# Optimization experiments

Measured on AMD Instinct MI355X. Metric: run time of the kernel, lower is better.

Reference implementation:

```python
import jax, jax.numpy as jnp
import numpy as np

THRESH = 0.33
EPS = 1e-10


def _ternarize(x, max_val):
    # x / (max(|x|)+eps) thresholded to {-1, 0, +1}
    n = x / (max_val + EPS)
    return jnp.where(n > THRESH, 1, jnp.where(n < -THRESH, -1, 0)).astype(jnp.int32)


def setup_inputs() -> dict:
    key = jax.random.key(0)
    k1, k2 = jax.random.split(key)
    V, D = 131072, 1024
    qs = jax.random.normal(k1, (D,), dtype=jnp.float32)
    # embedding init: xavier-ish normal + small noise, then row-normalized (as in _initialize_embeddings)
    W = jax.random.normal(k2, (V, D), dtype=jnp.float32)
    W = W / jnp.linalg.norm(W, axis=1, keepdims=True)
    return {"quantum_state": qs, "embedding_weight": W, "top_k": 16}


def reference(quantum_state, embedding_weight, top_k):
    V, D = embedding_weight.shape
    # --- coarse pass: ternary quantization of query and full table ---
    t_state = _ternarize(quantum_state, jnp.max(jnp.abs(quantum_state)))          # [D]
    t_emb = _ternarize(embedding_weight,
                       jnp.max(jnp.abs(embedding_weight), axis=1, keepdims=True))  # [V,D]
    eq = (t_state[None, :] == t_emb)                                               # [V,D]
    # matches contribute +1, mismatches -0.5 (matches.sum - 0.5*mismatches.sum)
    ternary_sim = jnp.sum(jnp.where(eq, 1.0, -0.5), axis=1)                        # [V]
    k3 = min(top_k * 3, V)
    _, top_ternary_idx = jax.lax.top_k(ternary_sim, k3)                            # [k3]
    # --- refine pass: cosine similarity on candidates ---
    cand = embedding_weight[top_ternary_idx]                                       # [k3,D]
    q_n = quantum_state / (jnp.linalg.norm(quantum_state) + 1e-12)
    c_n = cand / (jnp.linalg.norm(cand, axis=1, keepdims=True) + 1e-12)
    refined = c_n @ q_n                                                            # [k3]
    top_scores, top_local = jax.lax.top_k(refined, top_k)                          # [top_k]
    top_global = top_ternary_idx[top_local]
    return top_scores, top_global
```

## Files before the change

### kernel.cpp

```cpp
#include <hip/hip_runtime.h>
#include <stdint.h>

#define VROWS 131072
#define DIM   1024
#define TTHRESH 0.33f
#define TEPS    1e-10f
#define KB_BLOCKS 2048
#define REG_BLOCKS 832
#define NSB   32
#define CAP   16384
#define CAPL  4096

#define MBOUND ((double)TTHRESH + 0x1p-26)

#define CTRS_OFF  1024
#define MATCH_OFF 4096
#define PART_OFF  (MATCH_OFF + 4 * VROWS)
#define KEYS_OFF  ((PART_OFF + 4 * NSB * 1025 + 7) & ~7)

typedef float f32x4 __attribute__((ext_vector_type(4)));

__device__ __forceinline__ float max4abs(f32x4 a) {
    return fmaxf(fmaxf(fabsf(a.x), fabsf(a.y)), fmaxf(fabsf(a.z), fabsf(a.w)));
}

__device__ __forceinline__ float boundary(float d) {
    double md = MBOUND * (double)d;
    float r = (float)md;
    if (!((double)r >= md)) r = __int_as_float(__float_as_int(r) + 1);
    return r;
}

#define SLOT(x, j) { \
    unsigned long long bp = __ballot((x) >= r); \
    unsigned long long bn = __ballot((x) <= nr); \
    unsigned long long b0 = ~(bp | bn); \
    cnt += (int)__popcll((bp & MP[j]) | (bn & MN[j]) | (b0 & ~(MP[j] | MN[j]))); }

template <bool NT>
__device__ __forceinline__ f32x4 ldW(const f32x4* p) {
    if (NT) return __builtin_nontemporal_load(p);
    return *p;
}

template <bool NT>
__device__ __forceinline__ void rows16(const float* __restrict__ W, int row0, int lane,
                                       const unsigned long long* MP, const unsigned long long* MN,
                                       int* __restrict__ matches) {
    const f32x4* p = (const f32x4*)(W + (size_t)row0 * DIM) + lane;
    f32x4 c0 = ldW<NT>(p), c1 = ldW<NT>(p + 64), c2 = ldW<NT>(p + 128), c3 = ldW<NT>(p + 192);
    f32x4 n0 = c0, n1 = c1, n2 = c2, n3 = c3;
#pragma unroll 1
    for (int i = 0; i < 16; ++i) {
        if (i < 15) {
            const f32x4* pn = (const f32x4*)(W + (size_t)(row0 + i + 1) * DIM) + lane;
            n0 = ldW<NT>(pn); n1 = ldW<NT>(pn + 64); n2 = ldW<NT>(pn + 128); n3 = ldW<NT>(pn + 192);
        }
        float m = fmaxf(fmaxf(max4abs(c0), max4abs(c1)), fmaxf(max4abs(c2), max4abs(c3)));
        for (int s = 1; s < 64; s <<= 1) m = fmaxf(m, __shfl_xor(m, s));
        float r = boundary(m + TEPS), nr = -r;
        int cnt = 0;
        SLOT(c0.x, 0)  SLOT(c0.y, 1)  SLOT(c0.z, 2)  SLOT(c0.w, 3)
        SLOT(c1.x, 4)  SLOT(c1.y, 5)  SLOT(c1.z, 6)  SLOT(c1.w, 7)
        SLOT(c2.x, 8)  SLOT(c2.y, 9)  SLOT(c2.z, 10) SLOT(c2.w, 11)
        SLOT(c3.x, 12) SLOT(c3.y, 13) SLOT(c3.z, 14) SLOT(c3.w, 15)
        if (lane == 0) matches[row0 + i] = cnt;
        c0 = n0; c1 = n1; c2 = n2; c3 = n3;
    }
}

__global__ __launch_bounds__(256, 8) void kB_coarse(const float* __restrict__ W,
                                                    const float* __restrict__ q,
                                                    int* __restrict__ matches) {
    int t = threadIdx.x;
    int wave = t >> 6, lane = t & 63;

    const f32x4* q4 = (const f32x4*)q;
    f32x4 qv0 = q4[lane], qv1 = q4[64 + lane], qv2 = q4[128 + lane], qv3 = q4[192 + lane];
    float mq = fmaxf(fmaxf(max4abs(qv0), max4abs(qv1)), fmaxf(max4abs(qv2), max4abs(qv3)));
    for (int s = 1; s < 64; s <<= 1) mq = fmaxf(mq, __shfl_xor(mq, s));
    float rq = boundary(mq + TEPS), nrq = -rq;
    unsigned long long MP[16], MN[16];
#pragma unroll
    for (int j = 0; j < 4; ++j) {
        f32x4 v = (j == 0) ? qv0 : (j == 1) ? qv1 : (j == 2) ? qv2 : qv3;
        MP[j * 4 + 0] = __ballot(v.x >= rq);  MN[j * 4 + 0] = __ballot(v.x <= nrq);
        MP[j * 4 + 1] = __ballot(v.y >= rq);  MN[j * 4 + 1] = __ballot(v.y <= nrq);
        MP[j * 4 + 2] = __ballot(v.z >= rq);  MN[j * 4 + 2] = __ballot(v.z <= nrq);
        MP[j * 4 + 3] = __ballot(v.w >= rq);  MN[j * 4 + 3] = __ballot(v.w <= nrq);
    }

    int bb = (blockIdx.x * 997) & (KB_BLOCKS - 1);
    int row0 = bb * 64 + wave * 16;
    if (bb < REG_BLOCKS) {
        rows16<false>(W, row0, lane, MP, MN, matches);
    } else {
        rows16<true>(W, row0, lane, MP, MN, matches);
    }
}

__global__ __launch_bounds__(1024) void kHist(const int* __restrict__ matches,
                                              int* __restrict__ partials,
                                              int* __restrict__ ctrs) {
    __shared__ int h[1025];
    int t = threadIdx.x;
    if (t == 0) h[1024] = 0;
    if (blockIdx.x == 0 && t < 2) ctrs[t] = 0;
    h[t] = 0;
    __syncthreads();
    int gid = blockIdx.x * 1024 + t;
    int4 m4 = ((const int4*)matches)[gid];
    atomicAdd(&h[m4.x], 1);
    atomicAdd(&h[m4.y], 1);
    atomicAdd(&h[m4.z], 1);
    atomicAdd(&h[m4.w], 1);
    __syncthreads();
    int* dst = partials + blockIdx.x * 1025;
    dst[t] = h[t];
    if (t == 0) dst[1024] = h[1024];
}

__global__ __launch_bounds__(1024) void kGF(const float* __restrict__ W,
                                            const float* __restrict__ q,
                                            const int* __restrict__ topk,
                                            const int* __restrict__ matches,
                                            const int* __restrict__ partials,
                                            unsigned long long* __restrict__ keys,
                                            int* __restrict__ ctrs,
                                            float* __restrict__ out) {
    __shared__ int S[2048];
    __shared__ __align__(16) float qs[DIM];
    __shared__ float redf[1024];
    __shared__ unsigned long long kl[CAPL];
    __shared__ int sel[192];
    __shared__ float refined[192];
    __shared__ int sT, sWin, sG;
    __shared__ float sQn;
    int t = threadIdx.x;
    int b = blockIdx.x;
    int* gcount = &ctrs[0];
    int* done2 = &ctrs[1];

    int K = *topk;
    if (K < 1) K = 1;
    if (K > 64) K = 64;
    int k3 = 3 * K;
    if (k3 > VROWS) k3 = VROWS;

    int hb = 0, hb1 = 0;
    for (int k = 0; k < NSB; ++k) {
        hb += partials[k * 1025 + t];
        if (t == 0) hb1 += partials[k * 1025 + 1024];
    }
    S[t] = hb;
    S[1024 + t] = (t == 0) ? hb1 : 0;
    __syncthreads();

    for (int s = 1; s < 2048; s <<= 1) {
        int a = S[t] + ((t + s < 2048) ? S[t + s] : 0);
        int bsum = S[1024 + t] + ((1024 + t + s < 2048) ? S[1024 + t + s] : 0);
        __syncthreads();
        S[t] = a;
        S[1024 + t] = bsum;
        __syncthreads();
    }
    if (S[t] >= k3 && S[t + 1] < k3) sT = t;
    if (t == 0 && S[1024] >= k3) sT = 1024;
    __syncthreads();
    int T = sT;

    int gid = b * 1024 + t;
    int4 m4 = ((const int4*)matches)[gid];
    int rbase = gid * 4;
    if (m4.x >= T) { int p = atomicAdd(gcount, 1); if (p < CAP) keys[p] = ((unsigned long long)m4.x << 32) | (unsigned int)(~(rbase)); }
    if (m4.y >= T) { int p = atomicAdd(gcount, 1); if (p < CAP) keys[p] = ((unsigned long long)m4.y << 32) | (unsigned int)(~(rbase + 1)); }
    if (m4.z >= T) { int p = atomicAdd(gcount, 1); if (p < CAP) keys[p] = ((unsigned long long)m4.z << 32) | (unsigned int)(~(rbase + 2)); }
    if (m4.w >= T) { int p = atomicAdd(gcount, 1); if (p < CAP) keys[p] = ((unsigned long long)m4.w << 32) | (unsigned int)(~(rbase + 3)); }

    __threadfence();
    if (t == 0) sWin = atomicAdd(done2, 1);
    __syncthreads();
    if (sWin != NSB - 1) return;
    __threadfence();

    if (t < 256) ((float4*)qs)[t] = ((const float4*)q)[t];
    __syncthreads();
    float qv = qs[t];
    redf[t] = qv * qv;
    __syncthreads();
    for (int s = 512; s > 0; s >>= 1) {
        if (t < s) redf[t] += redf[t + s];
        __syncthreads();
    }
    if (t == 0) sQn = sqrtf(redf[0]) + 1e-12f;

    int G = atomicAdd(gcount, 0);
    if (G <= CAPL) {
        for (int i = t; i < G; i += 1024) kl[i] = keys[i];
        if (t == 0) sG = G;
    } else {
        if (t == 0) {
            int n = 0;
            for (int v = 0; v < VROWS && n < k3; ++v)
                if (matches[v] > T) kl[n++] = ((unsigned long long)matches[v] << 32) | (unsigned int)(~v);
            for (int v = 0; v < VROWS && n < k3; ++v)
                if (matches[v] == T) kl[n++] = ((unsigned long long)matches[v] << 32) | (unsigned int)(~v);
            sG = n;
        }
    }
    __syncthreads();
    G = sG;

    for (int i = t; i < G; i += 1024) {
        unsigned long long ki = kl[i];
        int rank = 0;
        for (int j = 0; j < G; ++j) rank += (kl[j] > ki) ? 1 : 0;
        if (rank < k3) sel[rank] = (int)(~(unsigned int)ki);
    }
    __syncthreads();

    int wave = t >> 6, lane = t & 63;
    float qn = sQn;
    for (int i = wave; i < k3; i += 16) {
        int row = sel[i];
        const float4* Wr = (const float4*)(W + (size_t)row * DIM);
        float dot = 0.f, ss = 0.f;
        for (int j2 = 0; j2 < 4; ++j2) {
            float4 a = Wr[j2 * 64 + lane];
            float4 bq = ((const float4*)qs)[j2 * 64 + lane];
            dot += a.x * bq.x + a.y * bq.y + a.z * bq.z + a.w * bq.w;
            ss  += a.x * a.x + a.y * a.y + a.z * a.z + a.w * a.w;
        }
        for (int s = 1; s < 64; s <<= 1) {
            dot += __shfl_xor(dot, s);
            ss  += __shfl_xor(ss, s);
        }
        if (lane == 0) refined[i] = dot / ((sqrtf(ss) + 1e-12f) * qn);
    }
    __syncthreads();

    if (t < k3) {
        float rv = refined[t];
        int rank = 0;
        for (int j = 0; j < k3; ++j)
            rank += ((refined[j] > rv) || (refined[j] == rv && j < t)) ? 1 : 0;
        if (rank < K) {
            out[rank] = rv;
            out[K + rank] = (float)sel[t];
        }
    }
}

extern "C" void kernel_launch(void* const* d_in, const int* in_sizes, int n_in,
                              void* d_out, int out_size, void* d_ws, size_t ws_size,
                              hipStream_t stream) {
    const float* q = (const float*)d_in[0];
    const float* W = (const float*)d_in[1];
    const int* topk = (const int*)d_in[2];
    float* out = (float*)d_out;
    char* ws = (char*)d_ws;

    int* ctrs = (int*)(ws + CTRS_OFF);
    int* matches = (int*)(ws + MATCH_OFF);
    int* partials = (int*)(ws + PART_OFF);
    unsigned long long* keys = (unsigned long long*)(ws + KEYS_OFF);

    kB_coarse<<<KB_BLOCKS, 256, 0, stream>>>(W, q, matches);
    kHist<<<NSB, 1024, 0, stream>>>(matches, partials, ctrs);
    kGF<<<NSB, 1024, 0, stream>>>(W, q, topk, matches, partials, keys, ctrs, out);
}
```

Before: 116.4 us.

## Use per-block local thresholds for candidate gathering; split final refine into its own kernel

Each histogram block now computes its own top-k3 threshold from its local histogram and gathers candidates directly. This removes the global partial-histogram reduction and the last-block-wins atomic election. The refine and top-k work moves to a separate single-block kernel that reads the gathered keys. A local threshold yields a superset of the true candidates, so the final rank step may process more keys (up to about 32·k3), and it falls back to ranking straight from global memory when the key count exceeds the LDS capacity.

```diff
diff --git a/kernel.cpp b/kernel.cpp
--- a/kernel.cpp
+++ b/kernel.cpp
@@ -15,8 +15,7 @@
 
 #define CTRS_OFF  1024
 #define MATCH_OFF 4096
-#define PART_OFF  (MATCH_OFF + 4 * VROWS)
-#define KEYS_OFF  ((PART_OFF + 4 * NSB * 1025 + 7) & ~7)
+#define KEYS_OFF  (MATCH_OFF + 4 * VROWS)
 
 typedef float f32x4 __attribute__((ext_vector_type(4)));
 
@@ -71,9 +70,11 @@
 
 __global__ __launch_bounds__(256, 8) void kB_coarse(const float* __restrict__ W,
                                                     const float* __restrict__ q,
-                                                    int* __restrict__ matches) {
+                                                    int* __restrict__ matches,
+                                                    int* __restrict__ ctrs) {
     int t = threadIdx.x;
     int wave = t >> 6, lane = t & 63;
+    if (blockIdx.x == 0 && t < 2) ctrs[t] = 0;
 
     const f32x4* q4 = (const f32x4*)q;
     f32x4 qv0 = q4[lane], qv1 = q4[64 + lane], qv2 = q4[128 + lane], qv3 = q4[192 + lane];
@@ -99,47 +100,81 @@
     }
 }
 
-__global__ __launch_bounds__(1024) void kHist(const int* __restrict__ matches,
-                                              int* __restrict__ partials,
-                                              int* __restrict__ ctrs) {
+__global__ __launch_bounds__(1024) void kLG(const int* __restrict__ matches,
+                                            const int* __restrict__ topk,
+                                            unsigned long long* __restrict__ keys,
+                                            int* __restrict__ gcount) {
     __shared__ int h[1025];
+    __shared__ int S[2048];
+    __shared__ int sT;
     int t = threadIdx.x;
+    int b = blockIdx.x;
+
+    int K = *topk;
+    if (K < 1) K = 1;
+    if (K > 64) K = 64;
+    int k3 = 3 * K;
+    if (k3 > VROWS) k3 = VROWS;
+
     if (t == 0) h[1024] = 0;
-    if (blockIdx.x == 0 && t < 2) ctrs[t] = 0;
     h[t] = 0;
     __syncthreads();
-    int gid = blockIdx.x * 1024 + t;
+    int gid = b * 1024 + t;
     int4 m4 = ((const int4*)matches)[gid];
     atomicAdd(&h[m4.x], 1);
     atomicAdd(&h[m4.y], 1);
     atomicAdd(&h[m4.z], 1);
     atomicAdd(&h[m4.w], 1);
     __syncthreads();
-    int* dst = partials + blockIdx.x * 1025;
-    dst[t] = h[t];
-    if (t == 0) dst[1024] = h[1024];
-}
-
-__global__ __launch_bounds__(1024) void kGF(const float* __restrict__ W,
-                                            const float* __restrict__ q,
-                                            const int* __restrict__ topk,
-                                            const int* __restrict__ matches,
-                                            const int* __restrict__ partials,
-                                            unsigned long long* __restrict__ keys,
-                                            int* __restrict__ ctrs,
-                                            float* __restrict__ out) {
-    __shared__ int S[2048];
+
+    S[t] = h[t];
+    S[1024 + t] = (t == 0) ? h[1024] : 0;
+    __syncthreads();
+    for (int s = 1; s < 2048; s <<= 1) {
+        int a = S[t] + ((t + s < 2048) ? S[t + s] : 0);
+        int bsum = S[1024 + t] + ((1024 + t + s < 2048) ? S[1024 + t + s] : 0);
+        __syncthreads();
+        S[t] = a;
+        S[1024 + t] = bsum;
+        __syncthreads();
+    }
+    if (S[t] >= k3 && S[t + 1] < k3) sT = t;
+    if (t == 0 && S[1024] >= k3) sT = 1024;
+    __syncthreads();
+    int T = sT;
+
+    int rbase = gid * 4;
+    if (m4.x >= T) { int p = atomicAdd(gcount, 1); if (p < CAP) keys[p] = ((unsigned long long)m4.x << 32) | (unsigned int)(~(rbase)); }
+    if (m4.y >= T) { int p = atomicAdd(gcount, 1); if (p < CAP) keys[p] = ((unsigned long long)m4.y << 32) | (unsigned int)(~(rbase + 1)); }
+    if (m4.z >= T) { int p = atomicAdd(gcount, 1); if (p < CAP) keys[p] = ((unsigned long long)m4.z << 32) | (unsigned int)(~(rbase + 2)); }
+    if (m4.w >= T) { int p = atomicAdd(gcount, 1); if (p < CAP) keys[p] = ((unsigned long long)m4.w << 32) | (unsigned int)(~(rbase + 3)); }
+}
+
+__global__ __launch_bounds__(1024) void kF_final(const float* __restrict__ W,
+                                                 const float* __restrict__ q,
+                                                 const int* __restrict__ topk,
+                                                 const unsigned long long* __restrict__ keys,
+                                                 const int* __restrict__ gcount,
+                                                 float* __restrict__ out) {
     __shared__ __align__(16) float qs[DIM];
     __shared__ float redf[1024];
     __shared__ unsigned long long kl[CAPL];
     __shared__ int sel[192];
     __shared__ float refined[192];
-    __shared__ int sT, sWin, sG;
     __shared__ float sQn;
     int t = threadIdx.x;
-    int b = blockIdx.x;
-    int* gcount = &ctrs[0];
-    int* done2 = &ctrs[1];
+
+    if (t < 256) ((float4*)qs)[t] = ((const float4*)q)[t];
+    __syncthreads();
+
+    float qv = qs[t];
+    redf[t] = qv * qv;
+    __syncthreads();
+    for (int s = 512; s > 0; s >>= 1) {
+        if (t < s) redf[t] += redf[t + s];
+        __syncthreads();
+    }
+    if (t == 0) sQn = sqrtf(redf[0]) + 1e-12f;
 
     int K = *topk;
     if (K < 1) K = 1;
@@ -147,75 +182,26 @@
     int k3 = 3 * K;
     if (k3 > VROWS) k3 = VROWS;
 
-    int hb = 0, hb1 = 0;
-    for (int k = 0; k < NSB; ++k) {
-        hb += partials[k * 1025 + t];
-        if (t == 0) hb1 += partials[k * 1025 + 1024];
-    }
-    S[t] = hb;
-    S[1024 + t] = (t == 0) ? hb1 : 0;
-    __syncthreads();
-
-    for (int s = 1; s < 2048; s <<= 1) {
-        int a = S[t] + ((t + s < 2048) ? S[t + s] : 0);
-        int bsum = S[1024 + t] + ((1024 + t + s < 2048) ? S[1024 + t + s] : 0);
-        __syncthreads();
-        S[t] = a;
-        S[1024 + t] = bsum;
-        __syncthreads();
-    }
-    if (S[t] >= k3 && S[t + 1] < k3) sT = t;
-    if (t == 0 && S[1024] >= k3) sT = 1024;
-    __syncthreads();
-    int T = sT;
-
-    int gid = b * 1024 + t;
-    int4 m4 = ((const int4*)matches)[gid];
-    int rbase = gid * 4;
-    if (m4.x >= T) { int p = atomicAdd(gcount, 1); if (p < CAP) keys[p] = ((unsigned long long)m4.x << 32) | (unsigned int)(~(rbase)); }
-    if (m4.y >= T) { int p = atomicAdd(gcount, 1); if (p < CAP) keys[p] = ((unsigned long long)m4.y << 32) | (unsigned int)(~(rbase + 1)); }
-    if (m4.z >= T) { int p = atomicAdd(gcount, 1); if (p < CAP) keys[p] = ((unsigned long long)m4.z << 32) | (unsigned int)(~(rbase + 2)); }
-    if (m4.w >= T) { int p = atomicAdd(gcount, 1); if (p < CAP) keys[p] = ((unsigned long long)m4.w << 32) | (unsigned int)(~(rbase + 3)); }
-
-    __threadfence();
-    if (t == 0) sWin = atomicAdd(done2, 1);
-    __syncthreads();
-    if (sWin != NSB - 1) return;
-    __threadfence();
-
-    if (t < 256) ((float4*)qs)[t] = ((const float4*)q)[t];
-    __syncthreads();
-    float qv = qs[t];
-    redf[t] = qv * qv;
-    __syncthreads();
-    for (int s = 512; s > 0; s >>= 1) {
-        if (t < s) redf[t] += redf[t + s];
-        __syncthreads();
-    }
-    if (t == 0) sQn = sqrtf(redf[0]) + 1e-12f;
-
-    int G = atomicAdd(gcount, 0);
+    int G = *gcount;
+    if (G > CAP) G = CAP;
+
     if (G <= CAPL) {
         for (int i = t; i < G; i += 1024) kl[i] = keys[i];
-        if (t == 0) sG = G;
+        __syncthreads();
+        for (int i = t; i < G; i += 1024) {
+            unsigned long long ki = kl[i];
+            int rank = 0;
+            for (int j = 0; j < G; ++j) rank += (kl[j] > ki) ? 1 : 0;
+            if (rank < k3) sel[rank] = (int)(~(unsigned int)ki);
+        }
     } else {
-        if (t == 0) {
-            int n = 0;
-            for (int v = 0; v < VROWS && n < k3; ++v)
-                if (matches[v] > T) kl[n++] = ((unsigned long long)matches[v] << 32) | (unsigned int)(~v);
-            for (int v = 0; v < VROWS && n < k3; ++v)
-                if (matches[v] == T) kl[n++] = ((unsigned long long)matches[v] << 32) | (unsigned int)(~v);
-            sG = n;
-        }
-    }
-    __syncthreads();
-    G = sG;
-
-    for (int i = t; i < G; i += 1024) {
-        unsigned long long ki = kl[i];
-        int rank = 0;
-        for (int j = 0; j < G; ++j) rank += (kl[j] > ki) ? 1 : 0;
-        if (rank < k3) sel[rank] = (int)(~(unsigned int)ki);
+        __syncthreads();
+        for (int i = t; i < G; i += 1024) {
+            unsigned long long ki = keys[i];
+            int rank = 0;
+            for (int j = 0; j < G; ++j) rank += (keys[j] > ki) ? 1 : 0;
+            if (rank < k3) sel[rank] = (int)(~(unsigned int)ki);
+        }
     }
     __syncthreads();
 
@@ -262,10 +248,9 @@
 
     int* ctrs = (int*)(ws + CTRS_OFF);
     int* matches = (int*)(ws + MATCH_OFF);
-    int* partials = (int*)(ws + PART_OFF);
     unsigned long long* keys = (unsigned long long*)(ws + KEYS_OFF);
 
-    kB_coarse<<<KB_BLOCKS, 256, 0, stream>>>(W, q, matches);
-    kHist<<<NSB, 1024, 0, stream>>>(matches, partials, ctrs);
-    kGF<<<NSB, 1024, 0, stream>>>(W, q, topk, matches, partials, keys, ctrs, out);
-}
+    kB_coarse<<<KB_BLOCKS, 256, 0, stream>>>(W, q, matches, ctrs);
+    kLG<<<NSB, 1024, 0, stream>>>(matches, topk, keys, &ctrs[0]);
+    kF_final<<<1, 1024, 0, stream>>>(W, q, topk, keys, &ctrs[0], out);
+}
```

New measurement: 174.7 us. +50.1%, slower.
